# Kernel optimization log

Measured on AMD Instinct MI355X. Metric: run time of the kernel, lower is better.

Reference implementation:

```python
import jax, jax.numpy as jnp
import numpy as np

B, N, D, K, H, L = 4, 20000, 64, 256, 4, 2
F = 4 * D
DH = D // H
SCALE = DH ** -0.5
EPS = 1e-5


def _layernorm(x, g, b):
    m = jnp.mean(x, axis=-1, keepdims=True)
    v = jnp.mean(jnp.square(x - m), axis=-1, keepdims=True)
    return (x - m) / jnp.sqrt(v + EPS) * g + b


def setup_inputs() -> dict:
    key = jax.random.key(0)
    ks = jax.random.split(key, 12)
    s = 0.02
    return {
        'expr': jax.random.normal(ks[0], (B, N), jnp.float32),
        'emb': jax.random.normal(ks[1], (N, D), jnp.float32),
        'Wq': jax.random.normal(ks[2], (L, D, D), jnp.float32) * s,
        'Wk': jax.random.normal(ks[3], (L, D, D), jnp.float32) * s,
        'Wv': jax.random.normal(ks[4], (L, D, D), jnp.float32) * s,
        'projK': jax.random.normal(ks[5], (L, N, K), jnp.float32) * s,
        'projV': jax.random.normal(ks[6], (L, N, K), jnp.float32) * s,
        'Wo': jax.random.normal(ks[7], (L, D, D), jnp.float32) * s,
        'bo': jnp.zeros((L, D), jnp.float32),
        'g1': jnp.ones((L, D), jnp.float32),
        'be1': jnp.zeros((L, D), jnp.float32),
        'W1': jax.random.normal(ks[8], (L, D, F), jnp.float32) * s,
        'bf1': jnp.zeros((L, F), jnp.float32),
        'W2': jax.random.normal(ks[9], (L, F, D), jnp.float32) * s,
        'bf2': jnp.zeros((L, D), jnp.float32),
        'g2': jnp.ones((L, D), jnp.float32),
        'be2': jnp.zeros((L, D), jnp.float32),
    }


def _forward(expr, emb, Wq, Wk, Wv, projK, projV, Wo, bo, g1, be1, W1, bf1, W2, bf2, g2, be2):
    # gene_ids = arange(N) for every batch row -> embedding lookup is just the table
    x = emb[None, :, :] * expr[:, :, None]  # [B, N, D]
    for i in range(L):
        b = x.shape[0]
        # Linformer self-attention
        q = jnp.einsum('bnd,de->bne', x, Wq[i])                 # [B, N, D]
        k_low = jnp.einsum('bnd,nk->bkd', x, projK[i])          # [B, K, D]
        v_low = jnp.einsum('bnd,nk->bkd', x, projV[i])          # [B, K, D]
        k = jnp.einsum('bkd,de->bke', k_low, Wk[i])             # [B, K, D]
        v = jnp.einsum('bkd,de->bke', v_low, Wv[i])             # [B, K, D]
        qh = q.reshape(b, N, H, DH).transpose(0, 2, 1, 3)       # [B, H, N, DH]
        kh = k.reshape(b, K, H, DH).transpose(0, 2, 1, 3)       # [B, H, K, DH]
        vh = v.reshape(b, K, H, DH).transpose(0, 2, 1, 3)       # [B, H, K, DH]
        dots = jnp.einsum('bhnd,bhkd->bhnk', qh, kh) * SCALE    # [B, H, N, K]
        attn = jax.nn.softmax(dots, axis=-1)
        o = jnp.einsum('bhnk,bhkd->bhnd', attn, vh)             # [B, H, N, DH]
        o = o.transpose(0, 2, 1, 3).reshape(b, N, D)
        o = jnp.einsum('bnd,de->bne', o, Wo[i]) + bo[i]
        x = _layernorm(o + x, g1[i], be1[i])
        # FFN (exact GELU, matching torch nn.GELU default)
        h = jax.nn.gelu(jnp.einsum('bnd,df->bnf', x, W1[i]) + bf1[i], approximate=False)
        f = jnp.einsum('bnf,fd->bnd', h, W2[i]) + bf2[i]
        x = _layernorm(f + x, g2[i], be2[i])
    return x


def reference(expr, emb, Wq, Wk, Wv, projK, projV, Wo, bo, g1, be1, W1, bf1, W2, bf2, g2, be2):
    return _forward(expr, emb, Wq, Wk, Wv, projK, projV, Wo, bo, g1, be1, W1, bf1, W2, bf2, g2, be2)
```

## Files before the change

kernel.cpp:

```cpp
#include <hip/hip_runtime.h>

using u16 = unsigned short;
typedef __bf16 bf16x8 __attribute__((ext_vector_type(8)));
typedef u16    u16x8  __attribute__((ext_vector_type(8)));
typedef u16    u16x4  __attribute__((ext_vector_type(4)));
typedef float  f32x4  __attribute__((ext_vector_type(4)));
typedef float  f32x16 __attribute__((ext_vector_type(16)));

#define DEV static __device__ __forceinline__

constexpr int NB = 4;
constexpr int NN = 20000;
constexpr int DD = 64;
constexpr int KK = 256;
constexpr int ROWS = NB * NN;

DEV float b2f(u16 u) { union { unsigned i; float f; } c; c.i = ((unsigned)u) << 16; return c.f; }
DEV u16 f2b(float f) {
  union { float f; unsigned i; } c; c.f = f;
  unsigned i = c.i + 0x7FFFu + ((c.i >> 16) & 1u);
  return (u16)(i >> 16);
}
DEV bf16x8 ldb8(const u16* p) { return *reinterpret_cast<const bf16x8*>(p); }
DEV f32x16 mfma32(bf16x8 a, bf16x8 b, f32x16 c) { return __builtin_amdgcn_mfma_f32_32x32x16_bf16(a, b, c, 0, 0, 0); }

__global__ __launch_bounds__(256) void k_wconv(
    const float* __restrict__ Wq, const float* __restrict__ Wo,
    const float* __restrict__ W1, const float* __restrict__ W2, u16* __restrict__ wb) {
  int m = blockIdx.y, l = blockIdx.z;
  const float* src; u16* dst; int Dout, S, CT;
  if (m == 0)      { src = Wq + l * 4096;  dst = wb + l * 4096;          Dout = 64;  S = 4;  CT = 2; }
  else if (m == 1) { src = Wo + l * 4096;  dst = wb + 8192 + l * 4096;   Dout = 64;  S = 4;  CT = 2; }
  else if (m == 2) { src = W1 + l * 16384; dst = wb + 16384 + l * 16384; Dout = 256; S = 4;  CT = 8; }
  else             { src = W2 + l * 16384; dst = wb + 49152 + l * 16384; Dout = 64;  S = 16; CT = 2; }
  int slot = blockIdx.x * 256 + threadIdx.x;
  if (slot >= S * CT * 64) return;
  int s = slot / (CT * 64), rem = slot % (CT * 64);
  int ct = rem >> 6, lane = rem & 63;
  int hi = lane >> 5, lo = lane & 31;
  u16x8 o;
#pragma unroll
  for (int j = 0; j < 8; ++j) o[j] = f2b(src[(s * 16 + hi * 8 + j) * Dout + ct * 32 + lo]);
  *reinterpret_cast<u16x8*>(&dst[slot * 8]) = o;
}

__global__ __launch_bounds__(256) void k_transpose(
    const float* __restrict__ projK, const float* __restrict__ projV,
    u16* __restrict__ pKT, u16* __restrict__ pVT) {
  int nt = blockIdx.x, kt = blockIdx.y, z = blockIdx.z;
  int layer = z & 1, pv = z >> 1;
  const float* src = (pv ? projV : projK) + (size_t)layer * NN * KK;
  u16* dst = (pv ? pVT : pKT) + (size_t)layer * KK * NN;
  int n0 = nt * 64, k0 = kt * 64;
  __shared__ float lds[64][65];
  int t = threadIdx.x;
  int r = t >> 4, c4 = (t & 15) * 4;
#pragma unroll
  for (int i = 0; i < 4; ++i) {
    int rr = r + i * 16;
    float4 v = make_float4(0.f, 0.f, 0.f, 0.f);
    if (n0 + rr < NN) v = *reinterpret_cast<const float4*>(&src[(size_t)(n0 + rr) * KK + k0 + c4]);
    lds[c4 + 0][rr] = v.x; lds[c4 + 1][rr] = v.y; lds[c4 + 2][rr] = v.z; lds[c4 + 3][rr] = v.w;
  }
  __syncthreads();
  int kr = t >> 3, nb = (t & 7) * 8;
#pragma unroll
  for (int p = 0; p < 2; ++p) {
    int k = kr + p * 32;
    if (n0 + nb < NN) {
      u16x8 o;
#pragma unroll
      for (int j = 0; j < 8; ++j) o[j] = f2b(lds[k][nb + j]);
      *reinterpret_cast<u16x8*>(&dst[(size_t)(k0 + k) * NN + n0 + nb]) = o;
    }
  }
}

__global__ __launch_bounds__(256) void k_xt(const u16* __restrict__ x, u16* __restrict__ xT) {
  int nt = blockIdx.x, b = blockIdx.y;
  int n0 = nt * 64;
  __shared__ u16 lds[64][70];
  int t = threadIdx.x;
  int r = t >> 4, c4 = (t & 15) * 4;
  const u16* xb = x + (size_t)b * NN * 64;
#pragma unroll
  for (int i = 0; i < 4; ++i) {
    int rr = r + i * 16;
    u16x4 v = {};
    if (n0 + rr < NN) v = *reinterpret_cast<const u16x4*>(&xb[(size_t)(n0 + rr) * 64 + c4]);
    lds[c4 + 0][rr] = v[0]; lds[c4 + 1][rr] = v[1];
    lds[c4 + 2][rr] = v[2]; lds[c4 + 3][rr] = v[3];
  }
  __syncthreads();
  int dr = t >> 3, nb = (t & 7) * 8;
  u16* xo = xT + (size_t)b * 64 * NN;
#pragma unroll
  for (int p = 0; p < 2; ++p) {
    int d = dr + p * 32;
    if (n0 + nb < NN) {
      u16x8 o;
#pragma unroll
      for (int j = 0; j < 8; ++j) o[j] = lds[d][nb + j];
      *reinterpret_cast<u16x8*>(&xo[(size_t)d * NN + n0 + nb]) = o;
    }
  }
}

__global__ __launch_bounds__(256) void k_embed(
    const float* __restrict__ expr, const float* __restrict__ emb, u16* __restrict__ xb) {
  int idx8 = (blockIdx.x * 256 + threadIdx.x) * 8;
  int b = idx8 / (NN * DD);
  int rem = idx8 - b * (NN * DD);
  int n = rem >> 6, d = rem & 63;
  float4 e0 = *reinterpret_cast<const float4*>(&emb[(n << 6) + d]);
  float4 e1 = *reinterpret_cast<const float4*>(&emb[(n << 6) + d + 4]);
  float s = expr[b * NN + n];
  u16x8 o;
  o[0] = f2b(e0.x * s); o[1] = f2b(e0.y * s); o[2] = f2b(e0.z * s); o[3] = f2b(e0.w * s);
  o[4] = f2b(e1.x * s); o[5] = f2b(e1.y * s); o[6] = f2b(e1.z * s); o[7] = f2b(e1.w * s);
  *reinterpret_cast<u16x8*>(&xb[idx8]) = o;
}

template <int EPI>
__global__ __launch_bounds__(256) void k_gemm_64_64(
    const u16* __restrict__ A, const u16* __restrict__ WB,
    const float* __restrict__ bias, const u16* __restrict__ res,
    const float* __restrict__ g, const float* __restrict__ be, u16* __restrict__ out) {
  int t = threadIdx.x, w = t >> 6, lane = t & 63;
  int lo = lane & 31, hi = lane >> 5;
  int unit = blockIdx.x * 4 + w;
  if (unit >= ROWS / 64) return;
  bf16x8 wf[4][2];
#pragma unroll
  for (int s = 0; s < 4; ++s)
#pragma unroll
    for (int ct = 0; ct < 2; ++ct) wf[s][ct] = ldb8(&WB[((s * 2 + ct) * 64 + lane) * 8]);
  float bia[2], gg[2], bb[2];
  if (EPI) {
#pragma unroll
    for (int ct = 0; ct < 2; ++ct) {
      bia[ct] = bias[ct * 32 + lo];
      gg[ct] = g[ct * 32 + lo];
      bb[ct] = be[ct * 32 + lo];
    }
  }
  f32x16 acc[2][2] = {};
  int r0 = unit * 64;
#pragma unroll
  for (int s = 0; s < 4; ++s) {
#pragma unroll
    for (int rt = 0; rt < 2; ++rt) {
      bf16x8 a = ldb8(&A[(size_t)(r0 + rt * 32 + lo) * 64 + s * 16 + hi * 8]);
      acc[rt][0] = mfma32(a, wf[s][0], acc[rt][0]);
      acc[rt][1] = mfma32(a, wf[s][1], acc[rt][1]);
    }
  }
#pragma unroll
  for (int rt = 0; rt < 2; ++rt) {
#pragma unroll
    for (int reg = 0; reg < 16; ++reg) {
      int row = r0 + rt * 32 + (reg & 3) + 8 * (reg >> 2) + 4 * hi;
      if (EPI == 0) {
        out[(size_t)row * 64 + lo] = f2b(acc[rt][0][reg]);
        out[(size_t)row * 64 + 32 + lo] = f2b(acc[rt][1][reg]);
      } else {
        float a0 = acc[rt][0][reg] + bia[0] + b2f(res[(size_t)row * 64 + lo]);
        float a1 = acc[rt][1][reg] + bia[1] + b2f(res[(size_t)row * 64 + 32 + lo]);
        float su = a0 + a1, sq = a0 * a0 + a1 * a1;
#pragma unroll
        for (int m = 1; m <= 16; m <<= 1) { su += __shfl_xor(su, m); sq += __shfl_xor(sq, m); }
        float mean = su * (1.f / 64.f);
        float var = sq * (1.f / 64.f) - mean * mean;
        float rstd = rsqrtf(var + 1e-5f);
        out[(size_t)row * 64 + lo] = f2b((a0 - mean) * rstd * gg[0] + bb[0]);
        out[(size_t)row * 64 + 32 + lo] = f2b((a1 - mean) * rstd * gg[1] + bb[1]);
      }
    }
  }
}

__global__ __launch_bounds__(256, 2) void k_gemm_64_256(
    const u16* __restrict__ A, const u16* __restrict__ WB,
    const float* __restrict__ bias, u16* __restrict__ out) {
  int t = threadIdx.x, w = t >> 6, lane = t & 63;
  int lo = lane & 31, hi = lane >> 5;
  int colg = w & 1;
  int unit = blockIdx.x * 2 + (w >> 1);
  if (unit >= ROWS / 32) return;
  bf16x8 wf[4][4];
  float bia[4];
#pragma unroll
  for (int s = 0; s < 4; ++s)
#pragma unroll
    for (int ct = 0; ct < 4; ++ct) wf[s][ct] = ldb8(&WB[((s * 8 + colg * 4 + ct) * 64 + lane) * 8]);
#pragma unroll
  for (int ct = 0; ct < 4; ++ct) bia[ct] = bias[colg * 128 + ct * 32 + lo];
  f32x16 acc[4] = {};
  int r0 = unit * 32;
#pragma unroll
  for (int s = 0; s < 4; ++s) {
    bf16x8 a = ldb8(&A[(size_t)(r0 + lo) * 64 + s * 16 + hi * 8]);
#pragma unroll
    for (int ct = 0; ct < 4; ++ct) acc[ct] = mfma32(a, wf[s][ct], acc[ct]);
  }
#pragma unroll
  for (int ct = 0; ct < 4; ++ct) {
#pragma unroll
    for (int reg = 0; reg < 16; ++reg) {
      int row = r0 + (reg & 3) + 8 * (reg >> 2) + 4 * hi;
      float x = acc[ct][reg] + bia[ct];
      float gel = 0.5f * x * (1.f + erff(x * 0.7071067811865475f));
      out[(size_t)row * 256 + colg * 128 + ct * 32 + lo] = f2b(gel);
    }
  }
}

__global__ __launch_bounds__(256) void k_gemm_256_64(
    const u16* __restrict__ A, const u16* __restrict__ WB,
    const float* __restrict__ bias, const u16* __restrict__ res,
    const float* __restrict__ g, const float* __restrict__ be,
    u16* __restrict__ outb, float* __restrict__ outf) {
  int t = threadIdx.x, w = t >> 6, lane = t & 63;
  int lo = lane & 31, hi = lane >> 5;
  int unit = blockIdx.x * 4 + w;
  if (unit >= ROWS / 64) return;
  float bia[2], gg[2], bb[2];
#pragma unroll
  for (int ct = 0; ct < 2; ++ct) {
    bia[ct] = bias[ct * 32 + lo];
    gg[ct] = g[ct * 32 + lo];
    bb[ct] = be[ct * 32 + lo];
  }
  f32x16 acc[2][2] = {};
  int r0 = unit * 64;
#pragma unroll
  for (int s = 0; s < 16; ++s) {
    bf16x8 w0 = ldb8(&WB[((s * 2 + 0) * 64 + lane) * 8]);
    bf16x8 w1 = ldb8(&WB[((s * 2 + 1) * 64 + lane) * 8]);
#pragma unroll
    for (int rt = 0; rt < 2; ++rt) {
      bf16x8 a = ldb8(&A[(size_t)(r0 + rt * 32 + lo) * 256 + s * 16 + hi * 8]);
      acc[rt][0] = mfma32(a, w0, acc[rt][0]);
      acc[rt][1] = mfma32(a, w1, acc[rt][1]);
    }
  }
#pragma unroll
  for (int rt = 0; rt < 2; ++rt) {
#pragma unroll
    for (int reg = 0; reg < 16; ++reg) {
      int row = r0 + rt * 32 + (reg & 3) + 8 * (reg >> 2) + 4 * hi;
      float a0 = acc[rt][0][reg] + bia[0] + b2f(res[(size_t)row * 64 + lo]);
      float a1 = acc[rt][1][reg] + bia[1] + b2f(res[(size_t)row * 64 + 32 + lo]);
      float su = a0 + a1, sq = a0 * a0 + a1 * a1;
#pragma unroll
      for (int m = 1; m <= 16; m <<= 1) { su += __shfl_xor(su, m); sq += __shfl_xor(sq, m); }
      float mean = su * (1.f / 64.f);
      float var = sq * (1.f / 64.f) - mean * mean;
      float rstd = rsqrtf(var + 1e-5f);
      float o0 = (a0 - mean) * rstd * gg[0] + bb[0];
      float o1 = (a1 - mean) * rstd * gg[1] + bb[1];
      if (outb) {
        outb[(size_t)row * 64 + lo] = f2b(o0);
        outb[(size_t)row * 64 + 32 + lo] = f2b(o1);
      }
      if (outf) {
        outf[(size_t)row * 64 + lo] = o0;
        outf[(size_t)row * 64 + 32 + lo] = o1;
      }
    }
  }
}

__global__ __launch_bounds__(256) void k_proj(
    const u16* __restrict__ xT, const u16* __restrict__ pKT_l, const u16* __restrict__ pVT_l,
    float* __restrict__ part) {
  int c = blockIdx.x, b = blockIdx.y, proj = blockIdx.z;
  const u16* P = proj ? pVT_l : pKT_l;
  int t = threadIdx.x, w = t >> 6, lane = t & 63;
  int lo = lane & 31, hi = lane >> 5;
  int d0 = (w & 1) * 32;
  int kbase = (w >> 1) * 128;
  int n0 = c * 512;
  int rem = NN - n0;
  int steps = (rem < 512 ? rem : 512) >> 4;
  const u16* xr = xT + ((size_t)b * 64 + d0 + lo) * NN;
  f32x16 acc[4] = {};
  for (int s = 0; s < steps; ++s) {
    int nb = n0 + s * 16 + hi * 8;
    bf16x8 a = ldb8(&xr[nb]);
#pragma unroll
    for (int gI = 0; gI < 4; ++gI) {
      bf16x8 bfr = ldb8(&P[(size_t)(kbase + gI * 32 + lo) * NN + nb]);
      acc[gI] = mfma32(a, bfr, acc[gI]);
    }
  }
  float* dst = part + ((size_t)(proj * NB + b) * 40 + c) * (64 * 256);
#pragma unroll
  for (int gI = 0; gI < 4; ++gI)
#pragma unroll
    for (int r = 0; r < 16; ++r) {
      int d = d0 + (r & 3) + 8 * (r >> 2) + 4 * hi;
      dst[d * 256 + kbase + gI * 32 + lo] = acc[gI][r];
    }
}

__global__ __launch_bounds__(256) void k_p2(
    const float* __restrict__ part, const float* __restrict__ Wk_l, const float* __restrict__ Wv_l,
    u16* __restrict__ kbuf, u16* __restrict__ vT) {
  int ks = blockIdx.x, b = blockIdx.y, proj = blockIdx.z;
  int k0 = ks * 8;
  const float* W = proj ? Wv_l : Wk_l;
  __shared__ float low[64][8];
  int t = threadIdx.x;
  const float* src = part + (size_t)(proj * NB + b) * 40 * (64 * 256);
#pragma unroll
  for (int i = 0; i < 2; ++i) {
    int idx = i * 256 + t;
    int e = idx >> 3, k = idx & 7;
    float s = 0.f;
    for (int cc = 0; cc < 40; ++cc) s += src[(size_t)cc * (64 * 256) + e * 256 + k0 + k];
    low[e][k] = s;
  }
  __syncthreads();
#pragma unroll
  for (int i = 0; i < 2; ++i) {
    int idx = i * 256 + t;
    int d = idx & 63, kk = idx >> 6;
    float a = 0.f;
#pragma unroll
    for (int e = 0; e < 64; ++e) a += low[e][kk] * W[e * 64 + d];
    u16 o = f2b(a);
    if (proj == 0)
      kbuf[((size_t)b * KK + k0 + kk) * 64 + d] = o;
    else
      vT[((size_t)b * 64 + d) * KK + k0 + kk] = o;
  }
}

__global__ __launch_bounds__(256) void k_attn(
    const u16* __restrict__ q, const u16* __restrict__ kbuf, const u16* __restrict__ vT,
    u16* __restrict__ ao) {
  int t = threadIdx.x, w = t >> 6, lane = t & 63;
  int lo = lane & 31, hi = lane >> 5;
  int h = blockIdx.y, b = blockIdx.z;
  int n0w = blockIdx.x * 128 + w * 32;
  if (n0w >= NN) return;
  const u16* qb = q + (size_t)b * NN * 64;
  const u16* kb = kbuf + (size_t)b * KK * 64 + h * 16;
  const u16* vtb = vT + (size_t)b * 64 * KK + (size_t)(h * 16 + (lane & 15)) * KK;
  u16* aob = ao + (size_t)b * NN * 64;
  const float C = 0.25f * 1.4426950408889634f;
  bf16x8 qf = ldb8(&qb[(size_t)(n0w + lo) * 64 + h * 16 + hi * 8]);
  f32x16 acc = {};
  float ssum = 0.f;
#pragma unroll
  for (int kt = 0; kt < 8; ++kt) {
    bf16x8 kf = ldb8(&kb[(size_t)(kt * 32 + lo) * 64 + hi * 8]);
    f32x16 z = {};
    f32x16 s = mfma32(kf, qf, z);
#pragma unroll
    for (int r = 0; r < 16; ++r) { s[r] = exp2f(s[r] * C); ssum += s[r]; }
#pragma unroll
    for (int c = 0; c < 2; ++c) {
      float px[8];
#pragma unroll
      for (int j = 0; j < 8; ++j) px[j] = __shfl_xor(s[c * 8 + j], 32);
      u16x8 bu;
#pragma unroll
      for (int j = 0; j < 4; ++j) {
        bu[j] = f2b(hi ? px[4 + j] : s[c * 8 + j]);
        bu[4 + j] = f2b(hi ? s[c * 8 + 4 + j] : px[j]);
      }
      bf16x8 af = ldb8(&vtb[kt * 32 + c * 16 + hi * 8]);
      acc = mfma32(af, __builtin_bit_cast(bf16x8, bu), acc);
    }
  }
  ssum += __shfl_xor(ssum, 32);
  float inv = 1.f / ssum;
  float o[8], ox[8];
#pragma unroll
  for (int r = 0; r < 8; ++r) o[r] = acc[r] * inv;
#pragma unroll
  for (int r = 0; r < 8; ++r) ox[r] = __shfl_xor(o[r], 32);
  u16x8 st;
#pragma unroll
  for (int j = 0; j < 4; ++j) {
    st[j] = f2b(hi ? ox[4 + j] : o[j]);
    st[4 + j] = f2b(hi ? o[4 + j] : ox[j]);
  }
  *reinterpret_cast<u16x8*>(&aob[(size_t)(n0w + lo) * 64 + h * 16 + hi * 8]) = st;
}

extern "C" void kernel_launch(void* const* d_in, const int* in_sizes, int n_in,
                              void* d_out, int out_size, void* d_ws, size_t ws_size,
                              hipStream_t stream) {
  const float* expr = (const float*)d_in[0];
  const float* emb  = (const float*)d_in[1];
  const float* Wq   = (const float*)d_in[2];
  const float* Wk   = (const float*)d_in[3];
  const float* Wv   = (const float*)d_in[4];
  const float* projK = (const float*)d_in[5];
  const float* projV = (const float*)d_in[6];
  const float* Wo   = (const float*)d_in[7];
  const float* bo   = (const float*)d_in[8];
  const float* g1   = (const float*)d_in[9];
  const float* be1  = (const float*)d_in[10];
  const float* W1   = (const float*)d_in[11];
  const float* bf1  = (const float*)d_in[12];
  const float* W2   = (const float*)d_in[13];
  const float* bf2  = (const float*)d_in[14];
  const float* g2   = (const float*)d_in[15];
  const float* be2  = (const float*)d_in[16];
  float* out = (float*)d_out;
  char* ws = (char*)d_ws;

  u16* xb0 = (u16*)(ws + 0);
  u16* xb1 = (u16*)(ws + 10240000);
  u16* xb2 = (u16*)(ws + 20480000);
  u16* qb  = (u16*)(ws + 30720000);
  u16* aob = (u16*)(ws + 40960000);
  u16* hb  = (u16*)(ws + 51200000);
  float* part = (float*)(ws + 51200000);
  u16* pKT = (u16*)(ws + 92160000);
  u16* pVT = (u16*)(ws + 112640000);
  u16* xTb = (u16*)(ws + 133120000);
  u16* kB  = (u16*)(ws + 143360000);
  u16* vTB = (u16*)(ws + 143491072);
  u16* wb  = (u16*)(ws + 143622144);

  k_wconv<<<dim3(8, 4, 2), 256, 0, stream>>>(Wq, Wo, W1, W2, wb);
  k_transpose<<<dim3(313, 4, 4), 256, 0, stream>>>(projK, projV, pKT, pVT);
  k_embed<<<2500, 256, 0, stream>>>(expr, emb, xb0);

  const u16* xin = xb0;
  for (int l = 0; l < 2; ++l) {
    const u16* wbq = wb + l * 4096;
    const u16* wbo = wb + 8192 + l * 4096;
    const u16* wb1 = wb + 16384 + l * 16384;
    const u16* wb2 = wb + 49152 + l * 16384;
    k_gemm_64_64<0><<<313, 256, 0, stream>>>(xin, wbq, nullptr, nullptr, nullptr, nullptr, qb);
    k_xt<<<dim3(313, NB), 256, 0, stream>>>(xin, xTb);
    k_proj<<<dim3(40, NB, 2), 256, 0, stream>>>(xTb, pKT + (size_t)l * KK * NN, pVT + (size_t)l * KK * NN, part);
    k_p2<<<dim3(32, NB, 2), 256, 0, stream>>>(part, Wk + l * 4096, Wv + l * 4096, kB, vTB);
    k_attn<<<dim3(157, 4, NB), 256, 0, stream>>>(qb, kB, vTB, aob);
    k_gemm_64_64<1><<<313, 256, 0, stream>>>(aob, wbo, bo + l * 64, xin, g1 + l * 64, be1 + l * 64, xb1);
    k_gemm_64_256<<<1250, 256, 0, stream>>>(xb1, wb1, bf1 + l * 256, hb);
    k_gemm_256_64<<<313, 256, 0, stream>>>(hb, wb2, bf2 + l * 64, xb1,
                                           g2 + l * 64, be2 + l * 64,
                                           l == 0 ? xb2 : nullptr, l == 1 ? out : nullptr);
    xin = xb2;
  }
}
```

Baseline: 490.4 us.

## Fold softmax scale into Wq, permute K rows to drop shuffles, split projection finer

```diff
diff --git a/kernel.cpp b/kernel.cpp
--- a/kernel.cpp
+++ b/kernel.cpp
@@ -6,6 +6,7 @@
 typedef u16    u16x4  __attribute__((ext_vector_type(4)));
 typedef float  f32x4  __attribute__((ext_vector_type(4)));
 typedef float  f32x16 __attribute__((ext_vector_type(16)));
+typedef unsigned u32x4 __attribute__((ext_vector_type(4)));
 
 #define DEV static __device__ __forceinline__
 
@@ -14,6 +15,7 @@
 constexpr int DD = 64;
 constexpr int KK = 256;
 constexpr int ROWS = NB * NN;
+constexpr int CH = 79;
 
 DEV float b2f(u16 u) { union { unsigned i; float f; } c; c.i = ((unsigned)u) << 16; return c.f; }
 DEV u16 f2b(float f) {
@@ -28,8 +30,9 @@
     const float* __restrict__ Wq, const float* __restrict__ Wo,
     const float* __restrict__ W1, const float* __restrict__ W2, u16* __restrict__ wb) {
   int m = blockIdx.y, l = blockIdx.z;
-  const float* src; u16* dst; int Dout, S, CT;
-  if (m == 0)      { src = Wq + l * 4096;  dst = wb + l * 4096;          Dout = 64;  S = 4;  CT = 2; }
+  const float* src; u16* dst; int Dout, S, CT; float sc = 1.f;
+  if (m == 0)      { src = Wq + l * 4096;  dst = wb + l * 4096;          Dout = 64;  S = 4;  CT = 2;
+                     sc = 0.25f * 1.4426950408889634f; }
   else if (m == 1) { src = Wo + l * 4096;  dst = wb + 8192 + l * 4096;   Dout = 64;  S = 4;  CT = 2; }
   else if (m == 2) { src = W1 + l * 16384; dst = wb + 16384 + l * 16384; Dout = 256; S = 4;  CT = 8; }
   else             { src = W2 + l * 16384; dst = wb + 49152 + l * 16384; Dout = 64;  S = 16; CT = 2; }
@@ -40,7 +43,7 @@
   int hi = lane >> 5, lo = lane & 31;
   u16x8 o;
 #pragma unroll
-  for (int j = 0; j < 8; ++j) o[j] = f2b(src[(s * 16 + hi * 8 + j) * Dout + ct * 32 + lo]);
+  for (int j = 0; j < 8; ++j) o[j] = f2b(sc * src[(s * 16 + hi * 8 + j) * Dout + ct * 32 + lo]);
   *reinterpret_cast<u16x8*>(&dst[slot * 8]) = o;
 }
 
@@ -271,7 +274,7 @@
   }
 }
 
-__global__ __launch_bounds__(256) void k_proj(
+__global__ __launch_bounds__(256, 3) void k_proj(
     const u16* __restrict__ xT, const u16* __restrict__ pKT_l, const u16* __restrict__ pVT_l,
     float* __restrict__ part) {
   int c = blockIdx.x, b = blockIdx.y, proj = blockIdx.z;
@@ -280,21 +283,35 @@
   int lo = lane & 31, hi = lane >> 5;
   int d0 = (w & 1) * 32;
   int kbase = (w >> 1) * 128;
-  int n0 = c * 512;
-  int rem = NN - n0;
-  int steps = (rem < 512 ? rem : 512) >> 4;
-  const u16* xr = xT + ((size_t)b * 64 + d0 + lo) * NN;
+  int n0 = c * 256;
+  const u16* xr = xT + ((size_t)b * 64 + d0 + lo) * NN + n0 + hi * 8;
+  const u16* pr0 = P + (size_t)(kbase + lo) * NN + n0 + hi * 8;
+  const u16* pr1 = pr0 + (size_t)32 * NN;
+  const u16* pr2 = pr0 + (size_t)64 * NN;
+  const u16* pr3 = pr0 + (size_t)96 * NN;
   f32x16 acc[4] = {};
-  for (int s = 0; s < steps; ++s) {
-    int nb = n0 + s * 16 + hi * 8;
-    bf16x8 a = ldb8(&xr[nb]);
-#pragma unroll
-    for (int gI = 0; gI < 4; ++gI) {
-      bf16x8 bfr = ldb8(&P[(size_t)(kbase + gI * 32 + lo) * NN + nb]);
-      acc[gI] = mfma32(a, bfr, acc[gI]);
-    }
-  }
-  float* dst = part + ((size_t)(proj * NB + b) * 40 + c) * (64 * 256);
+  if (n0 + 256 <= NN) {
+#pragma unroll
+    for (int s = 0; s < 16; ++s) {
+      int nb = s * 16;
+      bf16x8 a = ldb8(&xr[nb]);
+      acc[0] = mfma32(a, ldb8(&pr0[nb]), acc[0]);
+      acc[1] = mfma32(a, ldb8(&pr1[nb]), acc[1]);
+      acc[2] = mfma32(a, ldb8(&pr2[nb]), acc[2]);
+      acc[3] = mfma32(a, ldb8(&pr3[nb]), acc[3]);
+    }
+  } else {
+    int steps = (NN - n0) >> 4;
+    for (int s = 0; s < steps; ++s) {
+      int nb = s * 16;
+      bf16x8 a = ldb8(&xr[nb]);
+      acc[0] = mfma32(a, ldb8(&pr0[nb]), acc[0]);
+      acc[1] = mfma32(a, ldb8(&pr1[nb]), acc[1]);
+      acc[2] = mfma32(a, ldb8(&pr2[nb]), acc[2]);
+      acc[3] = mfma32(a, ldb8(&pr3[nb]), acc[3]);
+    }
+  }
+  float* dst = part + ((size_t)(proj * NB + b) * CH + c) * (64 * 256);
 #pragma unroll
   for (int gI = 0; gI < 4; ++gI)
 #pragma unroll
@@ -312,13 +329,13 @@
   const float* W = proj ? Wv_l : Wk_l;
   __shared__ float low[64][8];
   int t = threadIdx.x;
-  const float* src = part + (size_t)(proj * NB + b) * 40 * (64 * 256);
+  const float* src = part + (size_t)(proj * NB + b) * CH * (64 * 256);
 #pragma unroll
   for (int i = 0; i < 2; ++i) {
     int idx = i * 256 + t;
     int e = idx >> 3, k = idx & 7;
     float s = 0.f;
-    for (int cc = 0; cc < 40; ++cc) s += src[(size_t)cc * (64 * 256) + e * 256 + k0 + k];
+    for (int cc = 0; cc < CH; ++cc) s += src[(size_t)cc * (64 * 256) + e * 256 + k0 + k];
     low[e][k] = s;
   }
   __syncthreads();
@@ -330,10 +347,13 @@
 #pragma unroll
     for (int e = 0; e < 64; ++e) a += low[e][kk] * W[e * 64 + d];
     u16 o = f2b(a);
-    if (proj == 0)
-      kbuf[((size_t)b * KK + k0 + kk) * 64 + d] = o;
-    else
+    if (proj == 0) {
+      int key = k0 + kk;
+      int row = (key & ~12) | ((key & 4) << 1) | ((key & 8) >> 1);
+      kbuf[((size_t)b * KK + row) * 64 + d] = o;
+    } else {
       vT[((size_t)b * 64 + d) * KK + k0 + kk] = o;
+    }
   }
 }
 
@@ -349,7 +369,6 @@
   const u16* kb = kbuf + (size_t)b * KK * 64 + h * 16;
   const u16* vtb = vT + (size_t)b * 64 * KK + (size_t)(h * 16 + (lane & 15)) * KK;
   u16* aob = ao + (size_t)b * NN * 64;
-  const float C = 0.25f * 1.4426950408889634f;
   bf16x8 qf = ldb8(&qb[(size_t)(n0w + lo) * 64 + h * 16 + hi * 8]);
   f32x16 acc = {};
   float ssum = 0.f;
@@ -359,20 +378,18 @@
     f32x16 z = {};
     f32x16 s = mfma32(kf, qf, z);
 #pragma unroll
-    for (int r = 0; r < 16; ++r) { s[r] = exp2f(s[r] * C); ssum += s[r]; }
+    for (int r = 0; r < 16; ++r) { s[r] = exp2f(s[r]); ssum += s[r]; }
 #pragma unroll
     for (int c = 0; c < 2; ++c) {
-      float px[8];
-#pragma unroll
-      for (int j = 0; j < 8; ++j) px[j] = __shfl_xor(s[c * 8 + j], 32);
-      u16x8 bu;
-#pragma unroll
-      for (int j = 0; j < 4; ++j) {
-        bu[j] = f2b(hi ? px[4 + j] : s[c * 8 + j]);
-        bu[4 + j] = f2b(hi ? s[c * 8 + 4 + j] : px[j]);
+      u32x4 d;
+#pragma unroll
+      for (int i = 0; i < 4; ++i) {
+        unsigned a0 = __builtin_bit_cast(unsigned, s[c * 8 + 2 * i]) + 0x8000u;
+        unsigned a1 = __builtin_bit_cast(unsigned, s[c * 8 + 2 * i + 1]) + 0x8000u;
+        d[i] = __builtin_amdgcn_perm(a1, a0, 0x07060302u);
       }
       bf16x8 af = ldb8(&vtb[kt * 32 + c * 16 + hi * 8]);
-      acc = mfma32(af, __builtin_bit_cast(bf16x8, bu), acc);
+      acc = mfma32(af, __builtin_bit_cast(bf16x8, d), acc);
     }
   }
   ssum += __shfl_xor(ssum, 32);
@@ -420,13 +437,13 @@
   u16* qb  = (u16*)(ws + 30720000);
   u16* aob = (u16*)(ws + 40960000);
   u16* hb  = (u16*)(ws + 51200000);
-  float* part = (float*)(ws + 51200000);
   u16* pKT = (u16*)(ws + 92160000);
   u16* pVT = (u16*)(ws + 112640000);
   u16* xTb = (u16*)(ws + 133120000);
   u16* kB  = (u16*)(ws + 143360000);
   u16* vTB = (u16*)(ws + 143491072);
   u16* wb  = (u16*)(ws + 143622144);
+  float* part = (float*)(ws + 143786240);
 
   k_wconv<<<dim3(8, 4, 2), 256, 0, stream>>>(Wq, Wo, W1, W2, wb);
   k_transpose<<<dim3(313, 4, 4), 256, 0, stream>>>(projK, projV, pKT, pVT);
@@ -440,7 +457,7 @@
     const u16* wb2 = wb + 49152 + l * 16384;
     k_gemm_64_64<0><<<313, 256, 0, stream>>>(xin, wbq, nullptr, nullptr, nullptr, nullptr, qb);
     k_xt<<<dim3(313, NB), 256, 0, stream>>>(xin, xTb);
-    k_proj<<<dim3(40, NB, 2), 256, 0, stream>>>(xTb, pKT + (size_t)l * KK * NN, pVT + (size_t)l * KK * NN, part);
+    k_proj<<<dim3(CH, NB, 2), 256, 0, stream>>>(xTb, pKT + (size_t)l * KK * NN, pVT + (size_t)l * KK * NN, part);
     k_p2<<<dim3(32, NB, 2), 256, 0, stream>>>(part, Wk + l * 4096, Wv + l * 4096, kB, vTB);
     k_attn<<<dim3(157, 4, NB), 256, 0, stream>>>(qb, kB, vTB, aob);
     k_gemm_64_64<1><<<313, 256, 0, stream>>>(aob, wbo, bo + l * 64, xin, g1 + l * 64, be1 + l * 64, xb1);
```

New measurement: 523.6 us. +6.8%, slower.
